# Performance work log

Measured on AMD Instinct MI355X. Metric: run time of the kernel, lower is better.

The kernel has to match this reference:

```python
import jax, jax.numpy as jnp
import numpy as np

B, D, H1, H2 = 512, 1024, 512, 128

def setup_inputs() -> dict:
    key = jax.random.key(0)
    ks = jax.random.split(key, 3)
    x = jax.random.normal(ks[0], (B, D), dtype=jnp.float32)
    W1 = jax.random.normal(ks[1], (H1, D), dtype=jnp.float32)
    W2 = jax.random.normal(ks[2], (H2, H1), dtype=jnp.float32)
    b1 = jnp.full((H1,), 0.1, dtype=jnp.float32)
    b2 = jnp.full((H2,), 0.1, dtype=jnp.float32)
    b3 = jnp.full((H1,), 0.1, dtype=jnp.float32)
    b_r = jnp.full((D,), 0.1, dtype=jnp.float32)
    return {"x": x, "W1": W1, "b1": b1, "W2": W2, "b2": b2, "b3": b3, "b_r": b_r}

def reference(x, W1, b1, W2, b2, b3, b_r):
    # encoder
    c1 = jax.nn.sigmoid(x @ W1.T + b1)          # [B, H1]
    c2 = jax.nn.sigmoid(c1 @ W2.T + b2)         # [B, H2]
    # decoder (tied weights)
    c3 = jax.nn.sigmoid(c2 @ W2 + b3)           # [B, H1]
    recover = c3 @ W1 + b_r                     # [B, D]
    # Jacobian of code w.r.t. x, batched (replaces per-sample diag+matmul loop):
    # Jac[b] = diag(c2'(b)) @ W2 @ diag(c1'(b)) @ W1
    s1p = c1 * (1.0 - c1)                       # [B, H1]
    s2p = c2 * (1.0 - c2)                       # [B, H2]
    M = s2p[:, :, None] * W2[None, :, :] * s1p[:, None, :]   # [B, H2, H1]
    Jac = jnp.einsum('bhk,kd->bhd', M, W1)      # [B, H2, D]
    return (recover, c2, Jac)
```

## Files before the change

### kernel.cpp

```cpp
#include <hip/hip_runtime.h>


typedef _Float16 f16x8 __attribute__((ext_vector_type(8)));
typedef _Float16 f16x4 __attribute__((ext_vector_type(4)));
typedef float    f32x4 __attribute__((ext_vector_type(4)));
typedef float    f32x2 __attribute__((ext_vector_type(2)));

__device__ __forceinline__ void gld_lds16(const _Float16* src, _Float16* dst_wave_uniform) {
    __builtin_amdgcn_global_load_lds((const __attribute__((address_space(1))) unsigned int*)src,
                                     (__attribute__((address_space(3))) unsigned int*)dst_wave_uniform,
                                     16, 0, 0);
}

__device__ __forceinline__ void prep_dev(int bx, const float* __restrict__ W1,
                                         const float* __restrict__ W2,
                                         _Float16* __restrict__ W1T,
                                         _Float16* __restrict__ W2h) {
    if (bx < 512) {
        __shared__ float tile[32][33];
        int dt = (bx & 31) * 32, kt = (bx >> 5) * 32;
        int tx = threadIdx.x & 31, ty = threadIdx.x >> 5;
        #pragma unroll
        for (int r = 0; r < 32; r += 8)
            tile[ty + r][tx] = W1[(kt + ty + r) * 1024 + dt + tx];
        __syncthreads();
        #pragma unroll
        for (int r = 0; r < 32; r += 8)
            W1T[(size_t)(dt + ty + r) * 512 + kt + tx] = (_Float16)tile[tx][ty + r];
    } else {
        int i = (bx - 512) * 1024 + threadIdx.x * 4;
        f32x4 v = *(const f32x4*)(W2 + i);
        f16x4 h;
        h.x = (_Float16)v.x; h.y = (_Float16)v.y; h.z = (_Float16)v.z; h.w = (_Float16)v.w;
        *(f16x4*)(W2h + i) = h;
    }
}

template <int EPI, bool TRANSB>
__device__ void gemm_dev(const float* __restrict__ A, const float* __restrict__ Bm,
                         const float* __restrict__ bias,
                         float* __restrict__ C, float* __restrict__ Cd,
                         _Float16* __restrict__ Ch,
                         int M, int N, int K, int m0, int n0) {
    __shared__ __align__(16) float As[32][34];
    __shared__ __align__(16) float Bs[32][68];
    const int tid = threadIdx.x, tx = tid & 15, ty = tid >> 4;
    const int ka  = tid & 31, ma  = tid >> 5;
    const int kbt = tid & 31, nbt = tid >> 5;
    const int nbf = tid & 63, kbf = tid >> 6;
    float acc[2][4] = {};
    float rA[4], rB[8];

    #pragma unroll
    for (int r = 0; r < 4; ++r) rA[r] = A[(size_t)(m0 + ma + 8 * r) * K + ka];
    if (TRANSB) {
        #pragma unroll
        for (int r = 0; r < 8; ++r) rB[r] = Bm[(size_t)(n0 + nbt + 8 * r) * K + kbt];
    } else {
        #pragma unroll
        for (int r = 0; r < 8; ++r) rB[r] = Bm[(size_t)(kbf + 4 * r) * N + n0 + nbf];
    }

    for (int k0 = 0; k0 < K; k0 += 32) {
        #pragma unroll
        for (int r = 0; r < 4; ++r) As[ka][ma + 8 * r] = rA[r];
        if (TRANSB) {
            #pragma unroll
            for (int r = 0; r < 8; ++r) Bs[kbt][nbt + 8 * r] = rB[r];
        } else {
            #pragma unroll
            for (int r = 0; r < 8; ++r) Bs[kbf + 4 * r][nbf] = rB[r];
        }
        const int k1 = k0 + 32;
        if (k1 < K) {
            #pragma unroll
            for (int r = 0; r < 4; ++r) rA[r] = A[(size_t)(m0 + ma + 8 * r) * K + k1 + ka];
            if (TRANSB) {
                #pragma unroll
                for (int r = 0; r < 8; ++r) rB[r] = Bm[(size_t)(n0 + nbt + 8 * r) * K + k1 + kbt];
            } else {
                #pragma unroll
                for (int r = 0; r < 8; ++r) rB[r] = Bm[(size_t)(k1 + kbf + 4 * r) * N + n0 + nbf];
            }
        }
        __syncthreads();
        #pragma unroll
        for (int k = 0; k < 32; ++k) {
            f32x2 av = *(const f32x2*)&As[k][ty * 2];
            f32x4 bv = *(const f32x4*)&Bs[k][tx * 4];
            #pragma unroll
            for (int i = 0; i < 2; ++i)
                #pragma unroll
                for (int j = 0; j < 4; ++j)
                    acc[i][j] += av[i] * bv[j];
        }
        __syncthreads();
    }

    #pragma unroll
    for (int i = 0; i < 2; ++i) {
        int row = m0 + ty * 2 + i;
        #pragma unroll
        for (int j = 0; j < 4; ++j) {
            int col = n0 + tx * 4 + j;
            float z = acc[i][j] + bias[col];
            float s = 1.f / (1.f + __expf(-z));
            if constexpr (EPI == 1) {
                C[(size_t)row * N + col]  = s;
                Cd[(size_t)row * N + col] = s * (1.f - s);
            } else {
                Ch[(size_t)row * N + col] = (_Float16)s;
            }
        }
    }
}

__device__ __forceinline__ void buildA_dev(int b, const float* __restrict__ W2,
                                           const float* __restrict__ s1p,
                                           const float* __restrict__ s2p,
                                           _Float16* __restrict__ A_all) {
    const int tid = threadIdx.x;
    __shared__ float S1[512];
    __shared__ float S2[128];
    S1[tid]       = s1p[(size_t)b * 512 + tid];
    S1[tid + 256] = s1p[(size_t)b * 512 + tid + 256];
    if (tid < 128) S2[tid] = s2p[(size_t)b * 128 + tid];
    __syncthreads();
    _Float16* out = A_all + (size_t)b * 65536;
    #pragma unroll 4
    for (int i = 0; i < 32; ++i) {
        int c = tid + 256 * i;
        int h = c >> 6, k8 = (c & 63) * 8;
        f32x4 w0 = *(const f32x4*)(W2 + h * 512 + k8);
        f32x4 w1 = *(const f32x4*)(W2 + h * 512 + k8 + 4);
        float s2 = S2[h];
        f16x8 o;
        o[0] = (_Float16)(s2 * w0.x * S1[k8 + 0]);
        o[1] = (_Float16)(s2 * w0.y * S1[k8 + 1]);
        o[2] = (_Float16)(s2 * w0.z * S1[k8 + 2]);
        o[3] = (_Float16)(s2 * w0.w * S1[k8 + 3]);
        o[4] = (_Float16)(s2 * w1.x * S1[k8 + 4]);
        o[5] = (_Float16)(s2 * w1.y * S1[k8 + 5]);
        o[6] = (_Float16)(s2 * w1.z * S1[k8 + 6]);
        o[7] = (_Float16)(s2 * w1.w * S1[k8 + 7]);
        *(f16x8*)(out + h * 512 + k8) = o;
    }
}

__global__ __launch_bounds__(256) void fused_prep_gemm1(const float* __restrict__ x,
                                                        const float* __restrict__ W1,
                                                        const float* __restrict__ b1,
                                                        const float* __restrict__ W2,
                                                        _Float16* __restrict__ W1T,
                                                        _Float16* __restrict__ W2h,
                                                        float* __restrict__ c1,
                                                        float* __restrict__ s1p) {
    int bx = blockIdx.x;
    if (bx < 128) {
        gemm_dev<1, true>(x, W1, b1, c1, s1p, nullptr, 512, 512, 1024,
                          (bx >> 3) * 32, (bx & 7) * 64);
    } else {
        prep_dev(bx - 128, W1, W2, W1T, W2h);
    }
}

__global__ __launch_bounds__(256) void gemm2_kernel(const float* __restrict__ c1,
                                                    const float* __restrict__ W2,
                                                    const float* __restrict__ b2,
                                                    float* __restrict__ out_c2,
                                                    float* __restrict__ s2p) {
    gemm_dev<1, true>(c1, W2, b2, out_c2, s2p, nullptr, 512, 128, 512,
                      blockIdx.y * 32, blockIdx.x * 64);
}

__global__ __launch_bounds__(256) void gemm3_kernel(const float* __restrict__ out_c2,
                                                    const float* __restrict__ W2,
                                                    const float* __restrict__ b3,
                                                    _Float16* __restrict__ c3h) {
    gemm_dev<2, false>(out_c2, W2, b3, nullptr, nullptr, c3h, 512, 512, 128,
                       (blockIdx.x >> 3) * 32, (blockIdx.x & 7) * 64);
}

__global__ __launch_bounds__(256) void fused_mid(const float* __restrict__ out_c2,
                                                 const float* __restrict__ W2,
                                                 const float* __restrict__ b3,
                                                 _Float16* __restrict__ c3h,
                                                 const float* __restrict__ s1p,
                                                 const float* __restrict__ s2p,
                                                 _Float16* __restrict__ A_all) {
    int bx = blockIdx.x;
    if (bx < 128) {
        gemm_dev<2, false>(out_c2, W2, b3, nullptr, nullptr, c3h, 512, 512, 128,
                           (bx >> 3) * 32, (bx & 7) * 64);
    } else {
        buildA_dev(bx - 128, W2, s1p, s2p, A_all);
    }
}

__global__ __launch_bounds__(512, 2) void jac8_kernel(const _Float16* __restrict__ c3h,
                                                      const _Float16* __restrict__ A_all,
                                                      const _Float16* __restrict__ W1T,
                                                      const float* __restrict__ br,
                                                      float* __restrict__ out_rec,
                                                      float* __restrict__ out_jac) {
    __shared__ __align__(16) _Float16 Asl[2][256 * 64];
    __shared__ __align__(16) _Float16 Bsl[2][256 * 64];
    __shared__ float BiasS[256];

    const int bid = blockIdx.x;
    const _Float16* A;
    float* Out;
    int m0, n0;
    bool has_bias;
    if (bid < 8) {
        has_bias = true;
        A = c3h; Out = out_rec;
        m0 = (bid >> 2) * 256; n0 = (bid & 3) * 256;
    } else {
        int jid = bid - 8;
        int w = (jid & 7) * 128 + (jid >> 3);
        has_bias = false;
        A = A_all; Out = out_jac;
        m0 = (w >> 2) * 256; n0 = (w & 3) * 256;
    }

    const int tid = threadIdx.x;
    const int lane = tid & 63, wave = tid >> 6;
    const int wm = (wave >> 2) * 128, wn = (wave & 3) * 64;
    const int l15 = lane & 15, q = lane >> 4;

    if (tid < 256) BiasS[tid] = has_bias ? br[n0 + tid] : 0.f;

    const int srow = wave * 8 + (lane >> 3);
    const int skof = ((lane & 7) ^ (lane >> 3)) * 8;
    const _Float16* Abase = A   + (size_t)m0 * 512;
    const _Float16* Bbase = W1T + (size_t)n0 * 512;

    auto STAGE = [&](int t) {
        const int buf = t & 1;
        const int kb = t * 64;
        #pragma unroll
        for (int r = 0; r < 4; ++r)
            gld_lds16(Abase + (size_t)(r * 64 + srow) * 512 + kb + skof,
                      &Asl[buf][(r * 64 + wave * 8) * 64]);
        #pragma unroll
        for (int r = 0; r < 4; ++r)
            gld_lds16(Bbase + (size_t)(r * 64 + srow) * 512 + kb + skof,
                      &Bsl[buf][(r * 64 + wave * 8) * 64]);
    };

    f32x4 acc[8][4];
    #pragma unroll
    for (int i = 0; i < 8; ++i)
        #pragma unroll
        for (int j = 0; j < 4; ++j) acc[i][j] = (f32x4){0.f, 0.f, 0.f, 0.f};

    STAGE(0);
    STAGE(1);

    const int swz = (l15 & 7) * 8;

    #pragma unroll 1
    for (int t = 0; t < 8; ++t) {
        if (t < 7) asm volatile("s_waitcnt vmcnt(8)" ::: "memory");
        else       asm volatile("s_waitcnt vmcnt(0)" ::: "memory");
        __builtin_amdgcn_s_barrier();
        const int buf = t & 1;
        const _Float16* As = &Asl[buf][0];
        const _Float16* Bs = &Bsl[buf][0];

        f16x8 a0[8], b0[4];
        #pragma unroll
        for (int i = 0; i < 8; ++i)
            a0[i] = *(const f16x8*)(As + (wm + i * 16 + l15) * 64 + ((0 + q * 8) ^ swz));
        #pragma unroll
        for (int j = 0; j < 4; ++j)
            b0[j] = *(const f16x8*)(Bs + (wn + j * 16 + l15) * 64 + ((0 + q * 8) ^ swz));

        __builtin_amdgcn_s_setprio(1);
        #pragma unroll
        for (int i = 0; i < 8; ++i)
            #pragma unroll
            for (int j = 0; j < 4; ++j)
                acc[i][j] = __builtin_amdgcn_mfma_f32_16x16x32_f16(a0[i], b0[j], acc[i][j], 0, 0, 0);
        __builtin_amdgcn_s_setprio(0);

        f16x8 a1[8], b1[4];
        #pragma unroll
        for (int i = 0; i < 8; ++i)
            a1[i] = *(const f16x8*)(As + (wm + i * 16 + l15) * 64 + ((32 + q * 8) ^ swz));
        #pragma unroll
        for (int j = 0; j < 4; ++j)
            b1[j] = *(const f16x8*)(Bs + (wn + j * 16 + l15) * 64 + ((32 + q * 8) ^ swz));

        asm volatile("s_waitcnt lgkmcnt(0)" ::: "memory");
        __builtin_amdgcn_s_barrier();
        if (t + 2 < 8) STAGE(t + 2);
        __builtin_amdgcn_sched_barrier(0);

        __builtin_amdgcn_s_setprio(1);
        #pragma unroll
        for (int i = 0; i < 8; ++i)
            #pragma unroll
            for (int j = 0; j < 4; ++j)
                acc[i][j] = __builtin_amdgcn_mfma_f32_16x16x32_f16(a1[i], b1[j], acc[i][j], 0, 0, 0);
        __builtin_amdgcn_s_setprio(0);
    }

    #pragma unroll
    for (int i = 0; i < 8; ++i) {
        #pragma unroll
        for (int rg = 0; rg < 4; ++rg) {
            int m = m0 + wm + i * 16 + q * 4 + rg;
            #pragma unroll
            for (int j = 0; j < 4; ++j) {
                int col = wn + j * 16 + l15;
                Out[(size_t)m * 1024 + n0 + col] = acc[i][j][rg] + BiasS[col];
            }
        }
    }
}

template <bool HAS_BIAS>
__global__ __launch_bounds__(256) void mfma_bt(const _Float16* __restrict__ Abase,
                                               const _Float16* __restrict__ Bmat,
                                               const float* __restrict__ bias,
                                               float* __restrict__ OutBase,
                                               int K, int N,
                                               long aBatch, long oBatch) {
    __shared__ __align__(16) _Float16 Asl[128 * 64];
    __shared__ __align__(16) _Float16 Bsl[128 * 64];
    __shared__ float Bias[128];
    const _Float16* A = Abase + (size_t)blockIdx.z * aBatch;
    float* Out = OutBase + (size_t)blockIdx.z * oBatch;
    const int m0 = blockIdx.y * 128, n0 = blockIdx.x * 128;
    const int tid = threadIdx.x;
    const int lane = tid & 63, wave = tid >> 6;
    const int wm = (wave >> 1) * 64, wn = (wave & 1) * 64;
    const int l15 = lane & 15, q = lane >> 4;

    if (HAS_BIAS && tid < 128) Bias[tid] = bias[n0 + tid];

    f32x4 acc[4][4];
    #pragma unroll
    for (int i = 0; i < 4; ++i)
        #pragma unroll
        for (int j = 0; j < 4; ++j) acc[i][j] = (f32x4){0.f, 0.f, 0.f, 0.f};

    const int rbase = wave * 8 + (lane >> 3);
    const int kof   = (lane & 7) * 8;

    for (int k0 = 0; k0 < K; k0 += 64) {
        #pragma unroll
        for (int r = 0; r < 4; ++r) {
            gld_lds16(A    + (size_t)(m0 + r * 32 + rbase) * K + k0 + kof, Asl + (r * 32 + wave * 8) * 64);
            gld_lds16(Bmat + (size_t)(n0 + r * 32 + rbase) * K + k0 + kof, Bsl + (r * 32 + wave * 8) * 64);
        }
        __syncthreads();
        #pragma unroll
        for (int kk = 0; kk < 64; kk += 32) {
            f16x8 af[4], bf[4];
            #pragma unroll
            for (int i = 0; i < 4; ++i)
                af[i] = *(const f16x8*)(Asl + (wm + i * 16 + l15) * 64 + kk + q * 8);
            #pragma unroll
            for (int j = 0; j < 4; ++j)
                bf[j] = *(const f16x8*)(Bsl + (wn + j * 16 + l15) * 64 + kk + q * 8);
            #pragma unroll
            for (int i = 0; i < 4; ++i)
                #pragma unroll
                for (int j = 0; j < 4; ++j)
                    acc[i][j] = __builtin_amdgcn_mfma_f32_16x16x32_f16(af[i], bf[j], acc[i][j], 0, 0, 0);
        }
        __syncthreads();
    }

    #pragma unroll
    for (int i = 0; i < 4; ++i) {
        #pragma unroll
        for (int rg = 0; rg < 4; ++rg) {
            int m = m0 + wm + i * 16 + q * 4 + rg;
            #pragma unroll
            for (int j = 0; j < 4; ++j) {
                int dcol = wn + j * 16 + l15;
                float v = acc[i][j][rg];
                if (HAS_BIAS) v += Bias[dcol];
                Out[(size_t)m * N + n0 + dcol] = v;
            }
        }
    }
}

__global__ __launch_bounds__(256) void jac_kernel(const _Float16* __restrict__ W2h,
                                                  const _Float16* __restrict__ W1T,
                                                  const float* __restrict__ s1p,
                                                  const float* __restrict__ s2p,
                                                  float* __restrict__ Jac) {
    __shared__ __align__(16) _Float16 Asl[128 * 64];
    __shared__ __align__(16) _Float16 Bsl[128 * 64];
    __shared__ float Ssl[128];
    const int b  = blockIdx.y;
    const int n0 = blockIdx.x * 128;
    const int tid = threadIdx.x;
    const int lane = tid & 63, wave = tid >> 6;
    const int wm = (wave >> 1) * 64, wn = (wave & 1) * 64;
    const int l15 = lane & 15, q = lane >> 4;

    if (tid < 128) Ssl[tid] = s2p[b * 128 + tid];

    f32x4 acc[4][4];
    #pragma unroll
    for (int i = 0; i < 4; ++i)
        #pragma unroll
        for (int j = 0; j < 4; ++j) acc[i][j] = (f32x4){0.f, 0.f, 0.f, 0.f};

    const int ah  = tid >> 4;
    const int akq = (tid & 15) * 4;
    const int rbase = wave * 8 + (lane >> 3);
    const int kof   = (lane & 7) * 8;

    for (int k0 = 0; k0 < 512; k0 += 64) {
        f32x4 s4 = *(const f32x4*)(s1p + (size_t)b * 512 + k0 + akq);
        f16x4 s4h;
        s4h.x = (_Float16)s4.x; s4h.y = (_Float16)s4.y;
        s4h.z = (_Float16)s4.z; s4h.w = (_Float16)s4.w;
        #pragma unroll
        for (int r = 0; r < 8; ++r) {
            int h = ah + r * 16;
            f16x4 w4 = *(const f16x4*)(W2h + (size_t)h * 512 + k0 + akq);
            *(f16x4*)(Asl + h * 64 + akq) = w4 * s4h;
        }
        #pragma unroll
        for (int r = 0; r < 4; ++r)
            gld_lds16(W1T + (size_t)(n0 + r * 32 + rbase) * 512 + k0 + kof,
                      Bsl + (r * 32 + wave * 8) * 64);
        __syncthreads();

        #pragma unroll
        for (int kk = 0; kk < 64; kk += 32) {
            f16x8 af[4], bf[4];
            #pragma unroll
            for (int i = 0; i < 4; ++i)
                af[i] = *(const f16x8*)(Asl + (wm + i * 16 + l15) * 64 + kk + q * 8);
            #pragma unroll
            for (int j = 0; j < 4; ++j)
                bf[j] = *(const f16x8*)(Bsl + (wn + j * 16 + l15) * 64 + kk + q * 8);
            #pragma unroll
            for (int i = 0; i < 4; ++i)
                #pragma unroll
                for (int j = 0; j < 4; ++j)
                    acc[i][j] = __builtin_amdgcn_mfma_f32_16x16x32_f16(af[i], bf[j], acc[i][j], 0, 0, 0);
        }
        __syncthreads();
    }

    float* outb = Jac + (size_t)b * (128 * 1024);
    #pragma unroll
    for (int i = 0; i < 4; ++i) {
        #pragma unroll
        for (int rg = 0; rg < 4; ++rg) {
            int h = wm + i * 16 + q * 4 + rg;
            float s = Ssl[h];
            #pragma unroll
            for (int j = 0; j < 4; ++j) {
                int d = n0 + wn + j * 16 + l15;
                outb[(size_t)h * 1024 + d] = acc[i][j][rg] * s;
            }
        }
    }
}

extern "C" void kernel_launch(void* const* d_in, const int* in_sizes, int n_in,
                              void* d_out, int out_size, void* d_ws, size_t ws_size,
                              hipStream_t stream) {
    const float* x  = (const float*)d_in[0];
    const float* W1 = (const float*)d_in[1];
    const float* b1 = (const float*)d_in[2];
    const float* W2 = (const float*)d_in[3];
    const float* b2 = (const float*)d_in[4];
    const float* b3 = (const float*)d_in[5];
    const float* br = (const float*)d_in[6];

    float* out_rec = (float*)d_out;
    float* out_c2  = out_rec + 512 * 1024;
    float* out_jac = out_c2 + 512 * 128;

    char* ws = (char*)d_ws;
    _Float16* W1T   = (_Float16*)(ws);
    _Float16* W2h   = (_Float16*)(ws + 0x100000);
    float*    c1    = (float*)(ws + 0x120000);
    float*    s1p   = (float*)(ws + 0x220000);
    float*    s2p   = (float*)(ws + 0x320000);
    _Float16* c3h   = (_Float16*)(ws + 0x360000);
    _Float16* A_all = (_Float16*)(ws + 0x400000);
    const bool big_ws = ws_size >= (size_t)0x4400000;

    fused_prep_gemm1<<<704, 256, 0, stream>>>(x, W1, b1, W2, W1T, W2h, c1, s1p);
    gemm2_kernel<<<dim3(2, 16), 256, 0, stream>>>(c1, W2, b2, out_c2, s2p);
    if (big_ws) {
        fused_mid<<<640, 256, 0, stream>>>(out_c2, W2, b3, c3h, s1p, s2p, A_all);
        jac8_kernel<<<1032, 512, 0, stream>>>(c3h, A_all, W1T, br, out_rec, out_jac);
    } else {
        gemm3_kernel<<<128, 256, 0, stream>>>(out_c2, W2, b3, c3h);
        mfma_bt<true><<<dim3(8, 4, 1), 256, 0, stream>>>(c3h, W1T, br, out_rec, 512, 1024, 0, 0);
        jac_kernel<<<dim3(8, 512), 256, 0, stream>>>(W2h, W1T, s1p, s2p, out_jac);
    }
}
```

Before: 431.6 us.

## Halve jac8 K-slab to 32 with smaller LDS buffers and nontemporal output stores

The jac8 GEMM kernel now stages K in 32-wide slabs instead of 64-wide ones. That halves the LDS buffers from 128KB to 64KB, which likely allows two 512-thread blocks per CU as the launch bounds request. The loop now runs 16 iterations with one fragment load per step, and the swizzle and wait counts are adjusted to match. Output stores to the large Jacobian become nontemporal to avoid polluting the cache. The cost is more barriers per unit of work and less load/compute overlap within each iteration.

```diff
diff --git a/kernel.cpp b/kernel.cpp
--- a/kernel.cpp
+++ b/kernel.cpp
@@ -203,8 +203,8 @@
                                                       const float* __restrict__ br,
                                                       float* __restrict__ out_rec,
                                                       float* __restrict__ out_jac) {
-    __shared__ __align__(16) _Float16 Asl[2][256 * 64];
-    __shared__ __align__(16) _Float16 Bsl[2][256 * 64];
+    __shared__ __align__(16) _Float16 Asl[2][256 * 32];
+    __shared__ __align__(16) _Float16 Bsl[2][256 * 32];
     __shared__ float BiasS[256];
 
     const int bid = blockIdx.x;
@@ -231,22 +231,21 @@
 
     if (tid < 256) BiasS[tid] = has_bias ? br[n0 + tid] : 0.f;
 
-    const int srow = wave * 8 + (lane >> 3);
-    const int skof = ((lane & 7) ^ (lane >> 3)) * 8;
+    const int srow = lane >> 2;
+    const int skof = ((lane & 3) ^ ((lane >> 2) & 3)) * 8;
     const _Float16* Abase = A   + (size_t)m0 * 512;
     const _Float16* Bbase = W1T + (size_t)n0 * 512;
 
     auto STAGE = [&](int t) {
         const int buf = t & 1;
-        const int kb = t * 64;
-        #pragma unroll
-        for (int r = 0; r < 4; ++r)
-            gld_lds16(Abase + (size_t)(r * 64 + srow) * 512 + kb + skof,
-                      &Asl[buf][(r * 64 + wave * 8) * 64]);
-        #pragma unroll
-        for (int r = 0; r < 4; ++r)
-            gld_lds16(Bbase + (size_t)(r * 64 + srow) * 512 + kb + skof,
-                      &Bsl[buf][(r * 64 + wave * 8) * 64]);
+        const int kb = t * 32;
+        #pragma unroll
+        for (int r = 0; r < 2; ++r) {
+            gld_lds16(Abase + (size_t)(r * 128 + wave * 16 + srow) * 512 + kb + skof,
+                      &Asl[buf][(r * 128 + wave * 16) * 32]);
+            gld_lds16(Bbase + (size_t)(r * 128 + wave * 16 + srow) * 512 + kb + skof,
+                      &Bsl[buf][(r * 128 + wave * 16) * 32]);
+        }
     };
 
     f32x4 acc[8][4];
@@ -258,52 +257,37 @@
     STAGE(0);
     STAGE(1);
 
-    const int swz = (l15 & 7) * 8;
+    const int swz = l15 & 3;
 
     #pragma unroll 1
-    for (int t = 0; t < 8; ++t) {
-        if (t < 7) asm volatile("s_waitcnt vmcnt(8)" ::: "memory");
-        else       asm volatile("s_waitcnt vmcnt(0)" ::: "memory");
+    for (int t = 0; t < 16; ++t) {
+        if (t < 15) asm volatile("s_waitcnt vmcnt(4)" ::: "memory");
+        else        asm volatile("s_waitcnt vmcnt(0)" ::: "memory");
         __builtin_amdgcn_s_barrier();
         const int buf = t & 1;
         const _Float16* As = &Asl[buf][0];
         const _Float16* Bs = &Bsl[buf][0];
 
-        f16x8 a0[8], b0[4];
+        f16x8 af[8], bf[4];
         #pragma unroll
         for (int i = 0; i < 8; ++i)
-            a0[i] = *(const f16x8*)(As + (wm + i * 16 + l15) * 64 + ((0 + q * 8) ^ swz));
+            af[i] = *(const f16x8*)(As + (wm + i * 16 + l15) * 32 + (q ^ swz) * 8);
         #pragma unroll
         for (int j = 0; j < 4; ++j)
-            b0[j] = *(const f16x8*)(Bs + (wn + j * 16 + l15) * 64 + ((0 + q * 8) ^ swz));
+            bf[j] = *(const f16x8*)(Bs + (wn + j * 16 + l15) * 32 + (q ^ swz) * 8);
+
+        asm volatile("s_waitcnt lgkmcnt(0)" ::: "memory");
+        __builtin_amdgcn_sched_barrier(0);
+        __builtin_amdgcn_s_barrier();
+        if (t + 2 < 16) STAGE(t + 2);
+        __builtin_amdgcn_sched_barrier(0);
 
         __builtin_amdgcn_s_setprio(1);
         #pragma unroll
         for (int i = 0; i < 8; ++i)
             #pragma unroll
             for (int j = 0; j < 4; ++j)
-                acc[i][j] = __builtin_amdgcn_mfma_f32_16x16x32_f16(a0[i], b0[j], acc[i][j], 0, 0, 0);
-        __builtin_amdgcn_s_setprio(0);
-
-        f16x8 a1[8], b1[4];
-        #pragma unroll
-        for (int i = 0; i < 8; ++i)
-            a1[i] = *(const f16x8*)(As + (wm + i * 16 + l15) * 64 + ((32 + q * 8) ^ swz));
-        #pragma unroll
-        for (int j = 0; j < 4; ++j)
-            b1[j] = *(const f16x8*)(Bs + (wn + j * 16 + l15) * 64 + ((32 + q * 8) ^ swz));
-
-        asm volatile("s_waitcnt lgkmcnt(0)" ::: "memory");
-        __builtin_amdgcn_s_barrier();
-        if (t + 2 < 8) STAGE(t + 2);
-        __builtin_amdgcn_sched_barrier(0);
-
-        __builtin_amdgcn_s_setprio(1);
-        #pragma unroll
-        for (int i = 0; i < 8; ++i)
-            #pragma unroll
-            for (int j = 0; j < 4; ++j)
-                acc[i][j] = __builtin_amdgcn_mfma_f32_16x16x32_f16(a1[i], b1[j], acc[i][j], 0, 0, 0);
+                acc[i][j] = __builtin_amdgcn_mfma_f32_16x16x32_f16(af[i], bf[j], acc[i][j], 0, 0, 0);
         __builtin_amdgcn_s_setprio(0);
     }
 
@@ -315,7 +299,8 @@
             #pragma unroll
             for (int j = 0; j < 4; ++j) {
                 int col = wn + j * 16 + l15;
-                Out[(size_t)m * 1024 + n0 + col] = acc[i][j][rg] + BiasS[col];
+                __builtin_nontemporal_store(acc[i][j][rg] + BiasS[col],
+                                            Out + (size_t)m * 1024 + n0 + col);
             }
         }
     }
```

Measured after the change: 461.1 us. 1.07x slower.
